# Kernel optimization log

Hardware: AMD Instinct MI355X
Metric: run time of the kernel (lower is better)

## Reference

```python
import jax, jax.numpy as jnp
import numpy as np

NUM_EMBEDDINGS = 1024
EMBEDDING_DIM = 256
COMMITMENT_COST = 0.25


def setup_inputs() -> dict:
    key = jax.random.key(0)
    k1, k2 = jax.random.split(key)
    inputs = jax.random.normal(k1, (32, EMBEDDING_DIM, 32, 32), dtype=jnp.float32)
    # torch init: uniform_(-1/K, 1/K)
    emb_w = jax.random.uniform(k2, (NUM_EMBEDDINGS, EMBEDDING_DIM), dtype=jnp.float32,
                               minval=-1.0 / NUM_EMBEDDINGS, maxval=1.0 / NUM_EMBEDDINGS)
    return {"inputs": inputs, "emb_w": emb_w}


def reference(inputs, emb_w):
    sg = jax.lax.stop_gradient
    # BCHW -> BHWC
    x = jnp.transpose(inputs, (0, 2, 3, 1))
    in_shape = x.shape
    flat = x.reshape(-1, EMBEDDING_DIM)  # [N, D]
    # squared L2 distances to codebook: [N, K]
    distances = (jnp.sum(flat * flat, axis=1, keepdims=True)
                 + jnp.sum(emb_w * emb_w, axis=1)
                 - 2.0 * jnp.matmul(flat, emb_w.T))
    idx = jnp.argmin(distances, axis=1)  # [N]
    encodings = jax.nn.one_hot(idx, NUM_EMBEDDINGS, dtype=jnp.float32)  # [N, K]
    # one-hot @ codebook == gather
    quantized = jnp.take(emb_w, idx, axis=0).reshape(in_shape)  # [B,H,W,D]
    e_latent_loss = jnp.mean((sg(quantized) - x) ** 2)
    q_latent_loss = jnp.mean((quantized - sg(x)) ** 2)
    loss = q_latent_loss + COMMITMENT_COST * e_latent_loss
    # straight-through estimator
    quantized_st = x + sg(quantized - x)
    avg_probs = jnp.mean(encodings, axis=0)
    perplexity = jnp.exp(-jnp.sum(avg_probs * jnp.log(avg_probs + 1e-10)))
    return (loss, jnp.transpose(quantized_st, (0, 3, 1, 2)), perplexity, encodings)
```

## Files before the change

kernel.cpp:

```cpp
#include <hip/hip_runtime.h>
#include <hip/hip_bf16.h>

typedef short short8 __attribute__((ext_vector_type(8)));
typedef float f32x4 __attribute__((ext_vector_type(4)));
typedef unsigned short u16x4 __attribute__((ext_vector_type(4)));

#define D_ 256
#define K_ 1024
#define HW_ 1024
#define NROWS_ 32768
#define QELEMS 8388608

static __device__ __forceinline__ unsigned short to_bf16(float v) {
    __hip_bfloat16 h = __float2bfloat16(v);
    return *(unsigned short*)&h;
}

__global__ __launch_bounds__(256) void vq_prep(const float* __restrict__ emb,
    unsigned short* __restrict__ ebf, float* __restrict__ enorm,
    int* __restrict__ counts, double* __restrict__ loss_acc)
{
    int k = blockIdx.x, t = threadIdx.x;
    float v = emb[k * D_ + t];
    ebf[k * D_ + t] = to_bf16(v);
    float s = v * v;
    for (int o = 32; o > 0; o >>= 1) s += __shfl_down(s, o);
    __shared__ float ws4[4];
    if ((t & 63) == 0) ws4[t >> 6] = s;
    __syncthreads();
    if (t == 0) enorm[k] = ws4[0] + ws4[1] + ws4[2] + ws4[3];
    if (k < 4) counts[k * 256 + t] = 0;
    if (k == 0 && t == 0) *loss_acc = 0.0;
}

__global__ __launch_bounds__(512, 4) void vq_main(
    const float* __restrict__ x, const float* __restrict__ emb,
    const unsigned short* __restrict__ ebf, const float* __restrict__ enorm,
    int* __restrict__ counts, double* __restrict__ loss_acc, float* __restrict__ out)
{
    __shared__ char smem[66560];
    __shared__ float xn[64][33];
    __shared__ float rminv[64][4];
    __shared__ int   rmini[64][4];
    __shared__ int   bestsh[64];

    unsigned short* xs = (unsigned short*)smem;
    char* es = smem;

    const int t = threadIdx.x;
    const int n0 = blockIdx.x * 64;
    const int b = n0 >> 10;
    const int hw0 = n0 & 1023;
    const float* xbase = x + (size_t)b * (D_ * HW_) + hw0;

    {
        const int rt = t & 15;
        const int dg = t >> 4;
        const int r0 = rt * 4;
        float xp[4] = {0.f, 0.f, 0.f, 0.f};
#pragma unroll
        for (int m = 0; m < 2; ++m) {
            int d0 = (dg + 32 * m) * 4;
            f32x4 c[4];
#pragma unroll
            for (int q = 0; q < 4; ++q)
                c[q] = *(const f32x4*)(xbase + (size_t)(d0 + q) * HW_ + r0);
#pragma unroll
            for (int i = 0; i < 4; ++i) {
                u16x4 pk;
                pk[0] = to_bf16(c[0][i]); pk[1] = to_bf16(c[1][i]);
                pk[2] = to_bf16(c[2][i]); pk[3] = to_bf16(c[3][i]);
                xp[i] = fmaf(c[0][i], c[0][i], xp[i]);
                xp[i] = fmaf(c[1][i], c[1][i], xp[i]);
                xp[i] = fmaf(c[2][i], c[2][i], xp[i]);
                xp[i] = fmaf(c[3][i], c[3][i], xp[i]);
                int r = r0 + i;
                int byte = (r * 512 + d0 * 2) ^ ((r & 7) << 4);
                *(u16x4*)((char*)xs + byte) = pk;
            }
        }
#pragma unroll
        for (int i = 0; i < 4; ++i) xn[r0 + i][dg] = xp[i];
    }
    __syncthreads();

    const int lane = t & 63;
    const int w = t >> 6;
    const int rh = w & 1;
    const int cq = w >> 1;
    const int col = lane & 15;
    const int kg = lane >> 4;
    const char* ebf_bytes = (const char*)ebf;
    const int wbyte = w * 4096;

    {
#pragma unroll
        for (int j = 0; j < 4; ++j) {
            int p = wbyte + j * 1024 + lane * 16;
            int qq = p ^ (((p >> 9) & 7) << 4);
            __builtin_amdgcn_global_load_lds(ebf_bytes + qq, es + 32768 + wbyte + j * 1024, 16, 0, 0);
        }
    }

    short8 areg[2][8];
#pragma unroll
    for (int rt = 0; rt < 2; ++rt) {
        int row = rh * 32 + rt * 16 + col;
        int rowb = row * 512;
        int sw = (row & 7) << 4;
#pragma unroll
        for (int dc = 0; dc < 8; ++dc) {
            int byte = (rowb + dc * 64 + kg * 16) ^ sw;
            areg[rt][dc] = *(const short8*)((const char*)xs + byte);
        }
    }

    float v1[8]; int i1[8];
#pragma unroll
    for (int s = 0; s < 8; ++s) { v1[s] = 3.4e38f; i1[s] = 0x7fffffff; }

    for (int cc = 0; cc < 16; ++cc) {
        __syncthreads();
        const int hc = ((cc & 1) ^ 1) * 32768;
        if (cc < 15) {
            const char* src = ebf_bytes + (size_t)(cc + 1) * 32768;
            const int hn = (cc & 1) * 32768;
#pragma unroll
            for (int j = 0; j < 4; ++j) {
                int p = wbyte + j * 1024 + lane * 16;
                int qq = p ^ (((p >> 9) & 7) << 4);
                __builtin_amdgcn_global_load_lds(src + qq, es + hn + wbyte + j * 1024, 16, 0, 0);
            }
        }
        const int c0 = cq * 16 + col;
        const int sw0 = (c0 & 7) << 4;
        f32x4 acc0 = {0.f, 0.f, 0.f, 0.f};
        f32x4 acc1 = {0.f, 0.f, 0.f, 0.f};
#pragma unroll
        for (int dc = 0; dc < 8; ++dc) {
            short8 bf = *(const short8*)(es + hc + ((c0 * 512 + dc * 64 + kg * 16) ^ sw0));
            acc0 = __builtin_amdgcn_mfma_f32_16x16x32_bf16(areg[0][dc], bf, acc0, 0, 0, 0);
            acc1 = __builtin_amdgcn_mfma_f32_16x16x32_bf16(areg[1][dc], bf, acc1, 0, 0, 0);
        }
        int code = cc * 64 + c0;
        float bn = enorm[code];
#pragma unroll
        for (int r = 0; r < 4; ++r) {
            float dv = fmaf(-2.f, acc0[r], bn);
            if (dv < v1[r]) { v1[r] = dv; i1[r] = code; }
            float dw = fmaf(-2.f, acc1[r], bn);
            if (dw < v1[4 + r]) { v1[4 + r] = dw; i1[4 + r] = code; }
        }
    }

#pragma unroll
    for (int mask = 1; mask < 16; mask <<= 1) {
#pragma unroll
        for (int s = 0; s < 8; ++s) {
            float ov = __shfl_xor(v1[s], mask);
            int oi = __shfl_xor(i1[s], mask);
            if (ov < v1[s] || (ov == v1[s] && oi < i1[s])) { v1[s] = ov; i1[s] = oi; }
        }
    }
    if (col == 0) {
#pragma unroll
        for (int s = 0; s < 8; ++s) {
            int rt = s >> 2, r = s & 3;
            int row = rh * 32 + rt * 16 + kg * 4 + r;
            rminv[row][cq] = v1[s];
            rmini[row][cq] = i1[s];
        }
    }
    __syncthreads();

    if (t < 64) {
        float dmin = rminv[t][0]; int best = rmini[t][0];
#pragma unroll
        for (int g = 1; g < 4; ++g) {
            float cv = rminv[t][g]; int ci = rmini[t][g];
            if (cv < dmin || (cv == dmin && ci < best)) { dmin = cv; best = ci; }
        }
        bestsh[t] = best;
        atomicAdd(&counts[best], 1);
        float s = 0.f;
#pragma unroll 8
        for (int g = 0; g < 32; ++g) s += xn[t][g];
        float lrow = dmin + s;
        for (int o = 32; o > 0; o >>= 1) lrow += __shfl_down(lrow, o);
        if (t == 0) atomicAdd(loss_acc, (double)lrow);
    }
    __syncthreads();

    {
        int r = w * 8 + (lane & 7);
        int c = lane >> 3;
        const f32x4* src4 = (const f32x4*)emb + (size_t)bestsh[r] * 64 + c * 8;
        f32x4* dst4 = (f32x4*)smem + r * 65 + c * 8;
#pragma unroll
        for (int j = 0; j < 8; ++j) dst4[j] = src4[j];
    }
    __syncthreads();

    {
        const int hwr = t & 63;
        const int dq = t >> 6;
        float* outq = out + 1 + (size_t)b * (D_ * HW_) + hw0 + hwr;
        const float* qrow = (const float*)smem + hwr * 260;
#pragma unroll
        for (int dd = 0; dd < 32; ++dd) {
            int d = dq + dd * 8;
            outq[(size_t)d * HW_] = qrow[d];
        }
    }
    {
        float2* ez = (float2*)(out + 8388610 + (size_t)(n0 + w * 8) * 1024);
        float2 zz; zz.x = 0.f; zz.y = 0.f;
#pragma unroll 8
        for (int j = 0; j < 64; ++j) ez[j * 64 + lane] = zz;
    }
    __syncthreads();
    if (t < 64) out[8388610 + (size_t)(n0 + t) * 1024 + bestsh[t]] = 1.0f;
}

__global__ __launch_bounds__(256) void vq_fin(const int* __restrict__ counts,
    const double* __restrict__ loss_acc, float* __restrict__ d_out)
{
    int t = threadIdx.x;
    double s = 0.0;
    for (int k = t; k < K_; k += 256) {
        double p = (double)counts[k] / 32768.0;
        s += p * log(p + 1e-10);
    }
    for (int o = 32; o > 0; o >>= 1) s += __shfl_down(s, o);
    __shared__ double sred[4];
    if ((t & 63) == 0) sred[t >> 6] = s;
    __syncthreads();
    if (t == 0) {
        double tot = sred[0] + sred[1] + sred[2] + sred[3];
        d_out[0] = (float)(1.25 * (*loss_acc) / (double)QELEMS);
        d_out[8388609] = (float)exp(-tot);
    }
}

extern "C" void kernel_launch(void* const* d_in, const int* in_sizes, int n_in,
                              void* d_out, int out_size, void* d_ws, size_t ws_size,
                              hipStream_t stream)
{
    const float* x = (const float*)d_in[0];
    const float* emb = (const float*)d_in[1];
    char* ws = (char*)d_ws;
    unsigned short* ebf = (unsigned short*)(ws);
    float* enorm = (float*)(ws + 524288);
    int* counts = (int*)(ws + 528384);
    double* lacc = (double*)(ws + 532480);
    float* out = (float*)d_out;

    vq_prep<<<K_, 256, 0, stream>>>(emb, ebf, enorm, counts, lacc);
    vq_main<<<NROWS_ / 64, 512, 0, stream>>>(x, emb, ebf, enorm, counts, lacc, out);
    vq_fin<<<1, 256, 0, stream>>>(counts, lacc, out);
}
```

Baseline: 70.24 us.

## Fuse final reduction into main kernel and overlap one-hot zeroing with MFMA loop

The one-hot zero-fill stores move into the codebook chunk loop so the output writes overlap the MFMA distance computation instead of running afterwards. The separate finalization kernel is removed. A last-block-done atomic counter lets the final block compute perplexity and loss, saving one kernel launch. This adds a threadfence plus an atomic per block, and the in-loop stores may compete with the codebook global-to-LDS prefetch for memory bandwidth.

```diff
diff --git a/kernel.cpp b/kernel.cpp
--- a/kernel.cpp
+++ b/kernel.cpp
@@ -10,6 +10,7 @@
 #define HW_ 1024
 #define NROWS_ 32768
 #define QELEMS 8388608
+#define NBLK_ (NROWS_ / 64)
 
 static __device__ __forceinline__ unsigned short to_bf16(float v) {
     __hip_bfloat16 h = __float2bfloat16(v);
@@ -18,7 +19,7 @@
 
 __global__ __launch_bounds__(256) void vq_prep(const float* __restrict__ emb,
     unsigned short* __restrict__ ebf, float* __restrict__ enorm,
-    int* __restrict__ counts, double* __restrict__ loss_acc)
+    int* __restrict__ counts, double* __restrict__ loss_acc, int* __restrict__ done)
 {
     int k = blockIdx.x, t = threadIdx.x;
     float v = emb[k * D_ + t];
@@ -30,19 +31,22 @@
     __syncthreads();
     if (t == 0) enorm[k] = ws4[0] + ws4[1] + ws4[2] + ws4[3];
     if (k < 4) counts[k * 256 + t] = 0;
-    if (k == 0 && t == 0) *loss_acc = 0.0;
+    if (k == 0 && t == 0) { *loss_acc = 0.0; *done = 0; }
 }
 
 __global__ __launch_bounds__(512, 4) void vq_main(
     const float* __restrict__ x, const float* __restrict__ emb,
     const unsigned short* __restrict__ ebf, const float* __restrict__ enorm,
-    int* __restrict__ counts, double* __restrict__ loss_acc, float* __restrict__ out)
+    int* __restrict__ counts, double* __restrict__ loss_acc, int* __restrict__ done,
+    float* __restrict__ out)
 {
     __shared__ char smem[66560];
     __shared__ float xn[64][33];
     __shared__ float rminv[64][4];
     __shared__ int   rmini[64][4];
     __shared__ int   bestsh[64];
+    __shared__ double sred2[8];
+    __shared__ int lastflag;
 
     unsigned short* xs = (unsigned short*)smem;
     char* es = smem;
@@ -119,6 +123,9 @@
 #pragma unroll
     for (int s = 0; s < 8; ++s) { v1[s] = 3.4e38f; i1[s] = 0x7fffffff; }
 
+    float2* ezw = (float2*)(out + 8388610 + (size_t)(n0 + w * 8) * 1024);
+    const float2 zz2 = {0.f, 0.f};
+
     for (int cc = 0; cc < 16; ++cc) {
         __syncthreads();
         const int hc = ((cc & 1) ^ 1) * 32768;
@@ -131,6 +138,11 @@
                 int qq = p ^ (((p >> 9) & 7) << 4);
                 __builtin_amdgcn_global_load_lds(src + qq, es + hn + wbyte + j * 1024, 16, 0, 0);
             }
+        }
+        {
+            float2* ez = ezw + cc * 256;
+#pragma unroll
+            for (int j = 0; j < 4; ++j) ez[j * 64 + lane] = zz2;
         }
         const int c0 = cq * 16 + col;
         const int sw0 = (c0 & 7) << 4;
@@ -212,33 +224,35 @@
             outq[(size_t)d * HW_] = qrow[d];
         }
     }
-    {
-        float2* ez = (float2*)(out + 8388610 + (size_t)(n0 + w * 8) * 1024);
-        float2 zz; zz.x = 0.f; zz.y = 0.f;
-#pragma unroll 8
-        for (int j = 0; j < 64; ++j) ez[j * 64 + lane] = zz;
-    }
-    __syncthreads();
     if (t < 64) out[8388610 + (size_t)(n0 + t) * 1024 + bestsh[t]] = 1.0f;
-}
-
-__global__ __launch_bounds__(256) void vq_fin(const int* __restrict__ counts,
-    const double* __restrict__ loss_acc, float* __restrict__ d_out)
-{
-    int t = threadIdx.x;
-    double s = 0.0;
-    for (int k = t; k < K_; k += 256) {
-        double p = (double)counts[k] / 32768.0;
-        s += p * log(p + 1e-10);
-    }
-    for (int o = 32; o > 0; o >>= 1) s += __shfl_down(s, o);
-    __shared__ double sred[4];
-    if ((t & 63) == 0) sred[t >> 6] = s;
-    __syncthreads();
+    __syncthreads();
+
     if (t == 0) {
-        double tot = sred[0] + sred[1] + sred[2] + sred[3];
-        d_out[0] = (float)(1.25 * (*loss_acc) / (double)QELEMS);
-        d_out[8388609] = (float)exp(-tot);
+        __threadfence();
+        int old = atomicAdd(done, 1);
+        lastflag = (old == NBLK_ - 1) ? 1 : 0;
+    }
+    __syncthreads();
+    if (lastflag) {
+        double s = 0.0;
+#pragma unroll
+        for (int j = 0; j < 2; ++j) {
+            int k = t * 2 + j;
+            int cnt = __hip_atomic_load(&counts[k], __ATOMIC_RELAXED, __HIP_MEMORY_SCOPE_AGENT);
+            double p = (double)cnt / 32768.0;
+            s += p * log(p + 1e-10);
+        }
+        for (int o = 32; o > 0; o >>= 1) s += __shfl_down(s, o);
+        if (lane == 0) sred2[w] = s;
+        __syncthreads();
+        if (t == 0) {
+            double tot = 0.0;
+#pragma unroll
+            for (int g = 0; g < 8; ++g) tot += sred2[g];
+            double lw = __hip_atomic_load(loss_acc, __ATOMIC_RELAXED, __HIP_MEMORY_SCOPE_AGENT);
+            out[0] = (float)(1.25 * lw / (double)QELEMS);
+            out[8388609] = (float)exp(-tot);
+        }
     }
 }
 
@@ -253,9 +267,9 @@
     float* enorm = (float*)(ws + 524288);
     int* counts = (int*)(ws + 528384);
     double* lacc = (double*)(ws + 532480);
+    int* done = (int*)(ws + 532488);
     float* out = (float*)d_out;
 
-    vq_prep<<<K_, 256, 0, stream>>>(emb, ebf, enorm, counts, lacc);
-    vq_main<<<NROWS_ / 64, 512, 0, stream>>>(x, emb, ebf, enorm, counts, lacc, out);
-    vq_fin<<<1, 256, 0, stream>>>(counts, lacc, out);
-}
+    vq_prep<<<K_, 256, 0, stream>>>(emb, ebf, enorm, counts, lacc, done);
+    vq_main<<<NBLK_, 512, 0, stream>>>(x, emb, ebf, enorm, counts, lacc, done, out);
+}
```

Result: slower. 76.73 us (+9.2%).
